# Kernel optimization log

Hardware: AMD Instinct MI355X
Metric: run time of the kernel (lower is better)

The kernel has to match this reference:

```python
import jax, jax.numpy as jnp
import numpy as np

NOT_EPSILON = 1.0
B, S, D = 1, 512, 256


def swishmax(x, axis):
    xexp = x * jnp.exp(x - jnp.max(x, axis=axis, keepdims=True))
    return xexp / (jnp.sum(jnp.abs(xexp), axis=axis, keepdims=True) + NOT_EPSILON)


def setup_inputs() -> dict:
    key = jax.random.key(0)
    ks = jax.random.split(key, 13)
    scale = 1.0 / np.sqrt(D)
    mk = lambda k: jax.random.uniform(k, (D, D), jnp.float32, -scale, scale)
    mb = lambda k: jax.random.uniform(k, (D,), jnp.float32, -scale, scale)
    return {
        "query_tokens": jax.random.normal(ks[0], (B, S, D), jnp.float32),
        "key_tokens": jax.random.normal(ks[1], (B, S, D), jnp.float32),
        "value_tokens": jax.random.normal(ks[2], (B, S, D), jnp.float32),
        "Wk": mk(ks[3]), "bk": mb(ks[4]),
        "Wq": mk(ks[5]), "bq": mb(ks[6]),
        "Wva": mk(ks[7]), "bva": mb(ks[8]),
        "Wl": mk(ks[9]), "bl": mb(ks[10]),
        "Wvo": mk(ks[11]), "bvo": mb(ks[12]),
    }


def reference(query_tokens, key_tokens, value_tokens,
              Wk, bk, Wq, bq, Wva, bva, Wl, bl, Wvo, bvo):
    # residual linear transforms of tokens
    k = key_tokens + key_tokens @ Wk + bk        # [B,S,D]
    q = query_tokens + query_tokens @ Wq + bq    # [B,S,D]
    # batchify: key -> [B,Sk,1,D], query -> [B,1,Sq,D]; outer-product scores
    attention_raw = k[:, :, None, :] * q[:, None, :, :]          # [B,Sk,Sq,D]
    attention_logits = attention_raw + attention_raw @ Wl + bl   # DxD linear on raw scores
    attention_scale = swishmax(attention_logits, axis=-2)        # normalize over query axis (dim -shape_dims)
    v = value_tokens + value_tokens @ Wva + bva  # [B,S,D]
    values_scaled = v[:, :, None, :] * attention_scale           # [B,Sk,Sq,D]
    value_sum = values_scaled.sum(axis=-3)                       # reduce key axis -> [B,Sq,D]
    value_out = value_sum + value_sum @ Wvo + bvo
    return value_out
```

## Files before the change

### kernel.cpp

```cpp
#include <hip/hip_runtime.h>
#include <math.h>

#define S_LEN 512
#define D_DIM 256
#define SLICE (S_LEN * D_DIM)

#define LOG2E  1.44269504088896f
#define LN2    0.69314718055995f
#define C2     (8.0f * LOG2E)

#define EXP2F(x) __builtin_amdgcn_exp2f(x)

typedef _Float16 half8  __attribute__((ext_vector_type(8)));
typedef _Float16 half4v __attribute__((ext_vector_type(4)));
typedef float   floatx4 __attribute__((ext_vector_type(4)));

__global__ __launch_bounds__(256) void prep_wl(const float* __restrict__ Wl,
                                               _Float16* __restrict__ WlhT)
{
    const int d = blockIdx.x, e = threadIdx.x;
    float v = (Wl[e * D_DIM + d] + (e == d ? 1.0f : 0.0f)) * LOG2E;
    WlhT[d * D_DIM + e] = (_Float16)v;
}

__global__ __launch_bounds__(256) void linres3(
    const float* __restrict__ xk, const float* __restrict__ Wk,
    const float* __restrict__ bk, _Float16* __restrict__ yk16,
    const float* __restrict__ xq, const float* __restrict__ Wq,
    const float* __restrict__ bq, _Float16* __restrict__ yq16,
    const float* __restrict__ xv, const float* __restrict__ Wv,
    const float* __restrict__ bv, float* __restrict__ yv)
{
    __shared__ float xs[4][D_DIM];
    const int r0 = blockIdx.x * 4;
    const int sel = blockIdx.y;
    const float* x = sel == 0 ? xk : (sel == 1 ? xq : xv);
    const float* W = sel == 0 ? Wk : (sel == 1 ? Wq : Wv);
    const float* b = sel == 0 ? bk : (sel == 1 ? bq : bv);

    const int tid = threadIdx.x;
    #pragma unroll
    for (int t = 0; t < 4; ++t) xs[t][tid] = x[(r0 + t) * D_DIM + tid];
    __syncthreads();
    const float bv_ = b[tid];
    float acc[4];
    #pragma unroll
    for (int i = 0; i < 4; ++i) acc[i] = xs[i][tid] + bv_;
    #pragma unroll 4
    for (int e = 0; e < D_DIM; ++e) {
        const float w = W[e * D_DIM + tid];
        #pragma unroll
        for (int i = 0; i < 4; ++i) acc[i] += xs[i][e] * w;
    }
    if (sel == 2) {
        #pragma unroll
        for (int i = 0; i < 4; ++i) yv[(r0 + i) * D_DIM + tid] = acc[i];
    } else {
        _Float16* y16 = sel == 0 ? yk16 : yq16;
        #pragma unroll
        for (int i = 0; i < 4; ++i) y16[(r0 + i) * D_DIM + tid] = (_Float16)acc[i];
    }
}

__global__ __launch_bounds__(256) void linres_sum(
    const float* __restrict__ po, const float* __restrict__ W,
    const float* __restrict__ b, float* __restrict__ y)
{
    __shared__ float xs[4][D_DIM];
    const int tid = threadIdx.x;
    const int r0  = blockIdx.x * 4;
    #pragma unroll
    for (int t = 0; t < 4; ++t) {
        float s = 0.f;
        #pragma unroll
        for (int c = 0; c < 16; ++c)
            s += po[(size_t)c * SLICE + (r0 + t) * D_DIM + tid];
        xs[t][tid] = s;
    }
    __syncthreads();
    const float bv_ = b[tid];
    float acc[4];
    #pragma unroll
    for (int i = 0; i < 4; ++i) acc[i] = xs[i][tid] + bv_;
    #pragma unroll 4
    for (int e = 0; e < D_DIM; ++e) {
        const float w = W[e * D_DIM + tid];
        #pragma unroll
        for (int i = 0; i < 4; ++i) acc[i] += xs[i][e] * w;
    }
    #pragma unroll
    for (int i = 0; i < 4; ++i) y[(r0 + i) * D_DIM + tid] = acc[i];
}

__device__ __forceinline__ void stage_q(const _Float16* __restrict__ qh,
                                        _Float16* __restrict__ Afrag,
                                        int sq0, int tid)
{
    const int i   = tid & 63;
    const int qtr = tid >> 6;
    const int mt = i >> 4, l16 = i & 15;
    const half8* src = (const half8*)(qh + (size_t)(sq0 + i) * D_DIM + qtr * 64);
    #pragma unroll
    for (int u = 0; u < 8; ++u) {
        const int eb   = qtr * 8 + u;
        const int kk   = eb >> 2, quad = eb & 3;
        const int addr16 = (mt * 8 + kk) * 64 + quad * 16 + l16;
        *(half8*)(Afrag + addr16 * 8) = src[u];
    }
}

__device__ __forceinline__ void stage_q32(const _Float16* __restrict__ qh,
                                          _Float16* __restrict__ Afrag,
                                          int sq0, int tid)
{
    const int i   = tid & 31;
    const int oct = tid >> 5;
    const int mt = i >> 4, l16 = i & 15;
    const half8* src = (const half8*)(qh + (size_t)(sq0 + i) * D_DIM);
    #pragma unroll
    for (int u = 0; u < 4; ++u) {
        const int eb   = oct * 4 + u;
        const int kk   = eb >> 2, quad = eb & 3;
        const int addr16 = (mt * 8 + kk) * 64 + quad * 16 + l16;
        *(half8*)(Afrag + addr16 * 8) = src[eb];
    }
}

__global__ __launch_bounds__(256, 2) void stats_mfma(
    const _Float16* __restrict__ qh, const _Float16* __restrict__ kh,
    const _Float16* __restrict__ WlhT, const float* __restrict__ bl,
    float* __restrict__ pm, float* __restrict__ ps)
{
    __shared__ _Float16 Afrag[32 * 64 * 8];

    const int tid  = threadIdx.x;
    const int lane = tid & 63, wave = tid >> 6;
    const int quad = lane >> 4, l16 = lane & 15;
    const int sqt  = blockIdx.x, sq0 = sqt * 64;
    const int dw   = blockIdx.y * 128 + wave * 32;
    const int sk0  = blockIdx.z * 16;

    stage_q(qh, Afrag, sq0, tid);

    half8 wl[2][8];
    #pragma unroll
    for (int nt = 0; nt < 2; ++nt) {
        const int d = dw + nt * 16 + l16;
        #pragma unroll
        for (int kk = 0; kk < 8; ++kk)
            wl[nt][kk] = *(const half8*)(WlhT + (size_t)d * D_DIM + kk * 32 + quad * 8);
    }
    float bl_r[2];
    #pragma unroll
    for (int nt = 0; nt < 2; ++nt)
        bl_r[nt] = bl[dw + nt * 16 + l16] * LOG2E;

    __syncthreads();

    #pragma unroll 1
    for (int s = 0; s < 16; ++s) {
        const int sk = sk0 + s;
        floatx4 acc[4][2];
        #pragma unroll
        for (int mt = 0; mt < 4; ++mt)
            #pragma unroll
            for (int nt = 0; nt < 2; ++nt)
                acc[mt][nt] = (floatx4){0.f, 0.f, 0.f, 0.f};

        #pragma unroll
        for (int kk = 0; kk < 8; ++kk) {
            const half8 k8 = *(const half8*)(kh + (size_t)sk * D_DIM + kk * 32 + quad * 8);
            half8 af[4], bf[2];
            #pragma unroll
            for (int mt = 0; mt < 4; ++mt)
                af[mt] = *(const half8*)(Afrag + ((mt * 8 + kk) * 64 + lane) * 8);
            #pragma unroll
            for (int nt = 0; nt < 2; ++nt)
                bf[nt] = wl[nt][kk] * k8;
            #pragma unroll
            for (int mt = 0; mt < 4; ++mt)
                #pragma unroll
                for (int nt = 0; nt < 2; ++nt)
                    acc[mt][nt] = __builtin_amdgcn_mfma_f32_16x16x32_f16(
                        af[mt], bf[nt], acc[mt][nt], 0, 0, 0);
        }

        #pragma unroll
        for (int nt = 0; nt < 2; ++nt) {
            float mmx[4], tss[4];
            #pragma unroll
            for (int mt = 0; mt < 4; ++mt) {
                float L0 = acc[mt][nt][0] + bl_r[nt];
                float L1 = acc[mt][nt][1] + bl_r[nt];
                float L2 = acc[mt][nt][2] + bl_r[nt];
                float L3 = acc[mt][nt][3] + bl_r[nt];
                float t0 = fabsf(L0) * EXP2F(L0 - C2);
                float t1 = fabsf(L1) * EXP2F(L1 - C2);
                float t2 = fabsf(L2) * EXP2F(L2 - C2);
                float t3 = fabsf(L3) * EXP2F(L3 - C2);
                mmx[mt] = fmaxf(fmaxf(L0, L1), fmaxf(L2, L3));
                tss[mt] = (t0 + t1) + (t2 + t3);
            }
            float m  = fmaxf(fmaxf(mmx[0], mmx[1]), fmaxf(mmx[2], mmx[3]));
            float ss = (tss[0] + tss[1]) + (tss[2] + tss[3]);

            #pragma unroll
            for (int mask = 16; mask <= 32; mask <<= 1) {
                m  = fmaxf(m, __shfl_xor(m, mask, 64));
                ss += __shfl_xor(ss, mask, 64);
            }
            if (quad == 0) {
                const int d = dw + nt * 16 + l16;
                pm[((size_t)sqt * S_LEN + sk) * D_DIM + d] = m;
                ps[((size_t)sqt * S_LEN + sk) * D_DIM + d] = ss;
            }
        }
    }
}

__global__ __launch_bounds__(256) void reduce_ms(
    const float* __restrict__ pm, const float* __restrict__ ps,
    const float* __restrict__ vbuf, float* __restrict__ wbuf)
{
    const int idx = blockIdx.x * 256 + threadIdx.x;
    float mv[8], sv[8];
    #pragma unroll
    for (int t = 0; t < 8; ++t) {
        mv[t] = pm[(size_t)t * SLICE + idx];
        sv[t] = ps[(size_t)t * SLICE + idx];
    }
    float M = fmaxf(fmaxf(fmaxf(mv[0], mv[1]), fmaxf(mv[2], mv[3])),
                    fmaxf(fmaxf(mv[4], mv[5]), fmaxf(mv[6], mv[7])));
    float S = ((sv[0] + sv[1]) + (sv[2] + sv[3]))
            + ((sv[4] + sv[5]) + (sv[6] + sv[7]));
    const float denom = S * LN2 + EXP2F(M - C2);
    wbuf[idx] = vbuf[idx] * (LN2 / denom);
}

__global__ __launch_bounds__(256, 2) void accum_mfma(
    const _Float16* __restrict__ qh, const _Float16* __restrict__ kh,
    const _Float16* __restrict__ WlhT, const float* __restrict__ bl,
    const float* __restrict__ wbuf, float* __restrict__ po)
{
    __shared__ _Float16 Afrag[16 * 64 * 8];

    const int tid  = threadIdx.x;
    const int lane = tid & 63, wave = tid >> 6;
    const int quad = lane >> 4, l16 = lane & 15;
    const int sq0  = blockIdx.x * 32;
    const int dw   = blockIdx.y * 128 + wave * 32;
    const int chunk = blockIdx.z;
    const int sk0  = chunk * 32;

    stage_q32(qh, Afrag, sq0, tid);

    half8 wl[2][8];
    #pragma unroll
    for (int nt = 0; nt < 2; ++nt) {
        const int d = dw + nt * 16 + l16;
        #pragma unroll
        for (int kk = 0; kk < 8; ++kk)
            wl[nt][kk] = *(const half8*)(WlhT + (size_t)d * D_DIM + kk * 32 + quad * 8);
    }
    float bl_r[2];
    #pragma unroll
    for (int nt = 0; nt < 2; ++nt)
        bl_r[nt] = bl[dw + nt * 16 + l16] * LOG2E;

    __syncthreads();

    half8 afr[2][8];
    #pragma unroll
    for (int mt = 0; mt < 2; ++mt)
        #pragma unroll
        for (int kk = 0; kk < 8; ++kk)
            afr[mt][kk] = *(const half8*)(Afrag + ((mt * 8 + kk) * 64 + lane) * 8);

    floatx4 o[2][2];
    #pragma unroll
    for (int mt = 0; mt < 2; ++mt)
        #pragma unroll
        for (int nt = 0; nt < 2; ++nt)
            o[mt][nt] = (floatx4){0.f, 0.f, 0.f, 0.f};

    #pragma unroll 1
    for (int s = 0; s < 32; ++s) {
        const int sk = sk0 + s;

        float w_r2[2];
        #pragma unroll
        for (int nt = 0; nt < 2; ++nt)
            w_r2[nt] = wbuf[(size_t)sk * D_DIM + dw + nt * 16 + l16];

        floatx4 acc[2][2];
        #pragma unroll
        for (int mt = 0; mt < 2; ++mt)
            #pragma unroll
            for (int nt = 0; nt < 2; ++nt)
                acc[mt][nt] = (floatx4){0.f, 0.f, 0.f, 0.f};

        #pragma unroll
        for (int kk = 0; kk < 8; ++kk) {
            const half8 k8 = *(const half8*)(kh + (size_t)sk * D_DIM + kk * 32 + quad * 8);
            half8 bf[2];
            #pragma unroll
            for (int nt = 0; nt < 2; ++nt)
                bf[nt] = wl[nt][kk] * k8;
            #pragma unroll
            for (int mt = 0; mt < 2; ++mt)
                #pragma unroll
                for (int nt = 0; nt < 2; ++nt)
                    acc[mt][nt] = __builtin_amdgcn_mfma_f32_16x16x32_f16(
                        afr[mt][kk], bf[nt], acc[mt][nt], 0, 0, 0);
        }

        #pragma unroll
        for (int nt = 0; nt < 2; ++nt) {
            const float w_r = w_r2[nt];
            #pragma unroll
            for (int mt = 0; mt < 2; ++mt)
                #pragma unroll
                for (int r = 0; r < 4; ++r) {
                    const float L2 = acc[mt][nt][r] + bl_r[nt];
                    o[mt][nt][r] += w_r * (L2 * EXP2F(L2 - C2));
                }
        }
    }

    float* dst = po + (size_t)chunk * SLICE;
    #pragma unroll
    for (int mt = 0; mt < 2; ++mt)
        #pragma unroll
        for (int nt = 0; nt < 2; ++nt)
            #pragma unroll
            for (int r = 0; r < 4; ++r) {
                const int row = sq0 + mt * 16 + quad * 4 + r;
                const int col = dw + nt * 16 + l16;
                dst[(size_t)row * D_DIM + col] = o[mt][nt][r];
            }
}

extern "C" void kernel_launch(void* const* d_in, const int* in_sizes, int n_in,
                              void* d_out, int out_size, void* d_ws, size_t ws_size,
                              hipStream_t stream)
{
    const float* query = (const float*)d_in[0];
    const float* key   = (const float*)d_in[1];
    const float* value = (const float*)d_in[2];
    const float* Wk  = (const float*)d_in[3];
    const float* bk  = (const float*)d_in[4];
    const float* Wq  = (const float*)d_in[5];
    const float* bq  = (const float*)d_in[6];
    const float* Wva = (const float*)d_in[7];
    const float* bva = (const float*)d_in[8];
    const float* Wl  = (const float*)d_in[9];
    const float* bl  = (const float*)d_in[10];
    const float* Wvo = (const float*)d_in[11];
    const float* bvo = (const float*)d_in[12];

    const int MAT = SLICE;
    float* ws   = (float*)d_ws;
    float* vbuf = ws + 2 * MAT;
    float* wbuf = ws + 3 * MAT;
    _Float16* WlhT = (_Float16*)(ws + 6 * MAT);
    _Float16* kh   = (_Float16*)(ws + 6 * MAT + 32768);
    _Float16* qh   = kh + MAT;
    float* pm  = ws + 6 * MAT + 32768 + 2 * 65536;
    float* ps  = pm + 8 * MAT;
    float* po  = pm;
    float* out = (float*)d_out;

    prep_wl<<<256, 256, 0, stream>>>(Wl, WlhT);
    linres3<<<dim3(128, 3), 256, 0, stream>>>(key, Wk, bk, kh,
                                              query, Wq, bq, qh,
                                              value, Wva, bva, vbuf);

    stats_mfma<<<dim3(8, 2, 32), 256, 0, stream>>>(qh, kh, WlhT, bl, pm, ps);
    reduce_ms<<<512, 256, 0, stream>>>(pm, ps, vbuf, wbuf);
    accum_mfma<<<dim3(16, 2, 16), 256, 0, stream>>>(qh, kh, WlhT, bl,
                                                    wbuf, po);

    linres_sum<<<128, 256, 0, stream>>>(po, Wvo, bvo, out);
}
```

Baseline: 216.5 us.

## Fuse Wl prep into linres3, double key rows in stats, prefetch keys in accum

Merges the separate Wl transpose/convert kernel into the linres3 launch as an extra blockIdx.y slice, removing one launch. The stats kernel now processes two key rows per iteration so each LDS query fragment is reused across twice as many MFMAs. The accum kernel software-prefetches the next key row and weight values into registers while the current row's MFMAs and exp work run. It also changes the occupancy attributes, the unroll factors, and the linres_sum tiling (2 rows per block, 256 blocks). The trade-off is higher register pressure in the MFMA kernels.

```diff
diff --git a/kernel.cpp b/kernel.cpp
--- a/kernel.cpp
+++ b/kernel.cpp
@@ -14,14 +14,6 @@
 typedef _Float16 half8  __attribute__((ext_vector_type(8)));
 typedef _Float16 half4v __attribute__((ext_vector_type(4)));
 typedef float   floatx4 __attribute__((ext_vector_type(4)));
-
-__global__ __launch_bounds__(256) void prep_wl(const float* __restrict__ Wl,
-                                               _Float16* __restrict__ WlhT)
-{
-    const int d = blockIdx.x, e = threadIdx.x;
-    float v = (Wl[e * D_DIM + d] + (e == d ? 1.0f : 0.0f)) * LOG2E;
-    WlhT[d * D_DIM + e] = (_Float16)v;
-}
 
 __global__ __launch_bounds__(256) void linres3(
     const float* __restrict__ xk, const float* __restrict__ Wk,
@@ -29,16 +21,28 @@
     const float* __restrict__ xq, const float* __restrict__ Wq,
     const float* __restrict__ bq, _Float16* __restrict__ yq16,
     const float* __restrict__ xv, const float* __restrict__ Wv,
-    const float* __restrict__ bv, float* __restrict__ yv)
-{
+    const float* __restrict__ bv, float* __restrict__ yv,
+    const float* __restrict__ Wl, _Float16* __restrict__ WlhT)
+{
+    const int tid = threadIdx.x;
+    const int sel = blockIdx.y;
+
+    if (sel == 3) {
+        #pragma unroll
+        for (int t = 0; t < 2; ++t) {
+            const int d = blockIdx.x * 2 + t;
+            float v = (Wl[tid * D_DIM + d] + (tid == d ? 1.0f : 0.0f)) * LOG2E;
+            WlhT[d * D_DIM + tid] = (_Float16)v;
+        }
+        return;
+    }
+
     __shared__ float xs[4][D_DIM];
     const int r0 = blockIdx.x * 4;
-    const int sel = blockIdx.y;
     const float* x = sel == 0 ? xk : (sel == 1 ? xq : xv);
     const float* W = sel == 0 ? Wk : (sel == 1 ? Wq : Wv);
     const float* b = sel == 0 ? bk : (sel == 1 ? bq : bv);
 
-    const int tid = threadIdx.x;
     #pragma unroll
     for (int t = 0; t < 4; ++t) xs[t][tid] = x[(r0 + t) * D_DIM + tid];
     __syncthreads();
@@ -46,7 +50,7 @@
     float acc[4];
     #pragma unroll
     for (int i = 0; i < 4; ++i) acc[i] = xs[i][tid] + bv_;
-    #pragma unroll 4
+    #pragma unroll 8
     for (int e = 0; e < D_DIM; ++e) {
         const float w = W[e * D_DIM + tid];
         #pragma unroll
@@ -66,11 +70,11 @@
     const float* __restrict__ po, const float* __restrict__ W,
     const float* __restrict__ b, float* __restrict__ y)
 {
-    __shared__ float xs[4][D_DIM];
+    __shared__ float xs[2][D_DIM];
     const int tid = threadIdx.x;
-    const int r0  = blockIdx.x * 4;
-    #pragma unroll
-    for (int t = 0; t < 4; ++t) {
+    const int r0  = blockIdx.x * 2;
+    #pragma unroll
+    for (int t = 0; t < 2; ++t) {
         float s = 0.f;
         #pragma unroll
         for (int c = 0; c < 16; ++c)
@@ -79,17 +83,17 @@
     }
     __syncthreads();
     const float bv_ = b[tid];
-    float acc[4];
-    #pragma unroll
-    for (int i = 0; i < 4; ++i) acc[i] = xs[i][tid] + bv_;
-    #pragma unroll 4
+    float acc[2];
+    #pragma unroll
+    for (int i = 0; i < 2; ++i) acc[i] = xs[i][tid] + bv_;
+    #pragma unroll 8
     for (int e = 0; e < D_DIM; ++e) {
         const float w = W[e * D_DIM + tid];
         #pragma unroll
-        for (int i = 0; i < 4; ++i) acc[i] += xs[i][e] * w;
-    }
-    #pragma unroll
-    for (int i = 0; i < 4; ++i) y[(r0 + i) * D_DIM + tid] = acc[i];
+        for (int i = 0; i < 2; ++i) acc[i] += xs[i][e] * w;
+    }
+    #pragma unroll
+    for (int i = 0; i < 2; ++i) y[(r0 + i) * D_DIM + tid] = acc[i];
 }
 
 __device__ __forceinline__ void stage_q(const _Float16* __restrict__ qh,
@@ -126,7 +130,9 @@
     }
 }
 
-__global__ __launch_bounds__(256, 2) void stats_mfma(
+__global__ __launch_bounds__(256)
+__attribute__((amdgpu_waves_per_eu(2, 2)))
+void stats_mfma(
     const _Float16* __restrict__ qh, const _Float16* __restrict__ kh,
     const _Float16* __restrict__ WlhT, const float* __restrict__ bl,
     float* __restrict__ pm, float* __restrict__ ps)
@@ -158,63 +164,71 @@
     __syncthreads();
 
     #pragma unroll 1
-    for (int s = 0; s < 16; ++s) {
-        const int sk = sk0 + s;
-        floatx4 acc[4][2];
-        #pragma unroll
-        for (int mt = 0; mt < 4; ++mt)
-            #pragma unroll
-            for (int nt = 0; nt < 2; ++nt)
-                acc[mt][nt] = (floatx4){0.f, 0.f, 0.f, 0.f};
-
-        #pragma unroll
-        for (int kk = 0; kk < 8; ++kk) {
-            const half8 k8 = *(const half8*)(kh + (size_t)sk * D_DIM + kk * 32 + quad * 8);
-            half8 af[4], bf[2];
-            #pragma unroll
-            for (int mt = 0; mt < 4; ++mt)
-                af[mt] = *(const half8*)(Afrag + ((mt * 8 + kk) * 64 + lane) * 8);
-            #pragma unroll
-            for (int nt = 0; nt < 2; ++nt)
-                bf[nt] = wl[nt][kk] * k8;
+    for (int s2 = 0; s2 < 8; ++s2) {
+        const int sk = sk0 + s2 * 2;
+
+        floatx4 acc[2][4][2];
+        #pragma unroll
+        for (int c = 0; c < 2; ++c)
             #pragma unroll
             for (int mt = 0; mt < 4; ++mt)
                 #pragma unroll
                 for (int nt = 0; nt < 2; ++nt)
-                    acc[mt][nt] = __builtin_amdgcn_mfma_f32_16x16x32_f16(
-                        af[mt], bf[nt], acc[mt][nt], 0, 0, 0);
-        }
-
-        #pragma unroll
-        for (int nt = 0; nt < 2; ++nt) {
-            float mmx[4], tss[4];
+                    acc[c][mt][nt] = (floatx4){0.f, 0.f, 0.f, 0.f};
+
+        #pragma unroll
+        for (int kk = 0; kk < 8; ++kk) {
+            const half8 k8a = *(const half8*)(kh + (size_t)sk * D_DIM + kk * 32 + quad * 8);
+            const half8 k8b = *(const half8*)(kh + (size_t)(sk + 1) * D_DIM + kk * 32 + quad * 8);
+            half8 af[4];
+            #pragma unroll
+            for (int mt = 0; mt < 4; ++mt)
+                af[mt] = *(const half8*)(Afrag + ((mt * 8 + kk) * 64 + lane) * 8);
+            const half8 bfa0 = wl[0][kk] * k8a;
+            const half8 bfa1 = wl[1][kk] * k8a;
+            const half8 bfb0 = wl[0][kk] * k8b;
+            const half8 bfb1 = wl[1][kk] * k8b;
             #pragma unroll
             for (int mt = 0; mt < 4; ++mt) {
-                float L0 = acc[mt][nt][0] + bl_r[nt];
-                float L1 = acc[mt][nt][1] + bl_r[nt];
-                float L2 = acc[mt][nt][2] + bl_r[nt];
-                float L3 = acc[mt][nt][3] + bl_r[nt];
-                float t0 = fabsf(L0) * EXP2F(L0 - C2);
-                float t1 = fabsf(L1) * EXP2F(L1 - C2);
-                float t2 = fabsf(L2) * EXP2F(L2 - C2);
-                float t3 = fabsf(L3) * EXP2F(L3 - C2);
-                mmx[mt] = fmaxf(fmaxf(L0, L1), fmaxf(L2, L3));
-                tss[mt] = (t0 + t1) + (t2 + t3);
-            }
-            float m  = fmaxf(fmaxf(mmx[0], mmx[1]), fmaxf(mmx[2], mmx[3]));
-            float ss = (tss[0] + tss[1]) + (tss[2] + tss[3]);
-
-            #pragma unroll
-            for (int mask = 16; mask <= 32; mask <<= 1) {
-                m  = fmaxf(m, __shfl_xor(m, mask, 64));
-                ss += __shfl_xor(ss, mask, 64);
-            }
-            if (quad == 0) {
-                const int d = dw + nt * 16 + l16;
-                pm[((size_t)sqt * S_LEN + sk) * D_DIM + d] = m;
-                ps[((size_t)sqt * S_LEN + sk) * D_DIM + d] = ss;
+                acc[0][mt][0] = __builtin_amdgcn_mfma_f32_16x16x32_f16(af[mt], bfa0, acc[0][mt][0], 0, 0, 0);
+                acc[0][mt][1] = __builtin_amdgcn_mfma_f32_16x16x32_f16(af[mt], bfa1, acc[0][mt][1], 0, 0, 0);
+                acc[1][mt][0] = __builtin_amdgcn_mfma_f32_16x16x32_f16(af[mt], bfb0, acc[1][mt][0], 0, 0, 0);
+                acc[1][mt][1] = __builtin_amdgcn_mfma_f32_16x16x32_f16(af[mt], bfb1, acc[1][mt][1], 0, 0, 0);
             }
         }
+
+        #pragma unroll
+        for (int c = 0; c < 2; ++c)
+            #pragma unroll
+            for (int nt = 0; nt < 2; ++nt) {
+                float mmx[4], tss[4];
+                #pragma unroll
+                for (int mt = 0; mt < 4; ++mt) {
+                    float L0 = acc[c][mt][nt][0] + bl_r[nt];
+                    float L1 = acc[c][mt][nt][1] + bl_r[nt];
+                    float L2 = acc[c][mt][nt][2] + bl_r[nt];
+                    float L3 = acc[c][mt][nt][3] + bl_r[nt];
+                    float t0 = fabsf(L0) * EXP2F(L0 - C2);
+                    float t1 = fabsf(L1) * EXP2F(L1 - C2);
+                    float t2 = fabsf(L2) * EXP2F(L2 - C2);
+                    float t3 = fabsf(L3) * EXP2F(L3 - C2);
+                    mmx[mt] = fmaxf(fmaxf(L0, L1), fmaxf(L2, L3));
+                    tss[mt] = (t0 + t1) + (t2 + t3);
+                }
+                float m  = fmaxf(fmaxf(mmx[0], mmx[1]), fmaxf(mmx[2], mmx[3]));
+                float ss = (tss[0] + tss[1]) + (tss[2] + tss[3]);
+
+                #pragma unroll
+                for (int mask = 16; mask <= 32; mask <<= 1) {
+                    m  = fmaxf(m, __shfl_xor(m, mask, 64));
+                    ss += __shfl_xor(ss, mask, 64);
+                }
+                if (quad == 0) {
+                    const int d = dw + nt * 16 + l16;
+                    pm[((size_t)sqt * S_LEN + sk + c) * D_DIM + d] = m;
+                    ps[((size_t)sqt * S_LEN + sk + c) * D_DIM + d] = ss;
+                }
+            }
     }
 }
 
@@ -237,7 +251,9 @@
     wbuf[idx] = vbuf[idx] * (LN2 / denom);
 }
 
-__global__ __launch_bounds__(256, 2) void accum_mfma(
+__global__ __launch_bounds__(256)
+__attribute__((amdgpu_waves_per_eu(2, 2)))
+void accum_mfma(
     const _Float16* __restrict__ qh, const _Float16* __restrict__ kh,
     const _Float16* __restrict__ WlhT, const float* __restrict__ bl,
     const float* __restrict__ wbuf, float* __restrict__ po)
@@ -283,15 +299,17 @@
         for (int nt = 0; nt < 2; ++nt)
             o[mt][nt] = (floatx4){0.f, 0.f, 0.f, 0.f};
 
+    half8 k8c[8];
+    #pragma unroll
+    for (int kk = 0; kk < 8; ++kk)
+        k8c[kk] = *(const half8*)(kh + (size_t)sk0 * D_DIM + kk * 32 + quad * 8);
+    float w_c0 = wbuf[(size_t)sk0 * D_DIM + dw + l16];
+    float w_c1 = wbuf[(size_t)sk0 * D_DIM + dw + 16 + l16];
+
     #pragma unroll 1
     for (int s = 0; s < 32; ++s) {
         const int sk = sk0 + s;
 
-        float w_r2[2];
-        #pragma unroll
-        for (int nt = 0; nt < 2; ++nt)
-            w_r2[nt] = wbuf[(size_t)sk * D_DIM + dw + nt * 16 + l16];
-
         floatx4 acc[2][2];
         #pragma unroll
         for (int mt = 0; mt < 2; ++mt)
@@ -301,30 +319,32 @@
 
         #pragma unroll
         for (int kk = 0; kk < 8; ++kk) {
-            const half8 k8 = *(const half8*)(kh + (size_t)sk * D_DIM + kk * 32 + quad * 8);
-            half8 bf[2];
-            #pragma unroll
-            for (int nt = 0; nt < 2; ++nt)
-                bf[nt] = wl[nt][kk] * k8;
-            #pragma unroll
-            for (int mt = 0; mt < 2; ++mt)
-                #pragma unroll
-                for (int nt = 0; nt < 2; ++nt)
-                    acc[mt][nt] = __builtin_amdgcn_mfma_f32_16x16x32_f16(
-                        afr[mt][kk], bf[nt], acc[mt][nt], 0, 0, 0);
+            const half8 bf0 = wl[0][kk] * k8c[kk];
+            const half8 bf1 = wl[1][kk] * k8c[kk];
+            acc[0][0] = __builtin_amdgcn_mfma_f32_16x16x32_f16(afr[0][kk], bf0, acc[0][0], 0, 0, 0);
+            acc[0][1] = __builtin_amdgcn_mfma_f32_16x16x32_f16(afr[0][kk], bf1, acc[0][1], 0, 0, 0);
+            acc[1][0] = __builtin_amdgcn_mfma_f32_16x16x32_f16(afr[1][kk], bf0, acc[1][0], 0, 0, 0);
+            acc[1][1] = __builtin_amdgcn_mfma_f32_16x16x32_f16(afr[1][kk], bf1, acc[1][1], 0, 0, 0);
         }
 
-        #pragma unroll
-        for (int nt = 0; nt < 2; ++nt) {
-            const float w_r = w_r2[nt];
-            #pragma unroll
-            for (int mt = 0; mt < 2; ++mt)
-                #pragma unroll
-                for (int r = 0; r < 4; ++r) {
-                    const float L2 = acc[mt][nt][r] + bl_r[nt];
-                    o[mt][nt][r] += w_r * (L2 * EXP2F(L2 - C2));
-                }
+        const float w_use0 = w_c0, w_use1 = w_c1;
+        if (s < 31) {
+            #pragma unroll
+            for (int kk = 0; kk < 8; ++kk)
+                k8c[kk] = *(const half8*)(kh + (size_t)(sk + 1) * D_DIM + kk * 32 + quad * 8);
+            w_c0 = wbuf[(size_t)(sk + 1) * D_DIM + dw + l16];
+            w_c1 = wbuf[(size_t)(sk + 1) * D_DIM + dw + 16 + l16];
         }
+
+        #pragma unroll
+        for (int mt = 0; mt < 2; ++mt)
+            #pragma unroll
+            for (int r = 0; r < 4; ++r) {
+                const float La = acc[mt][0][r] + bl_r[0];
+                const float Lb = acc[mt][1][r] + bl_r[1];
+                o[mt][0][r] += w_use0 * (La * EXP2F(La - C2));
+                o[mt][1][r] += w_use1 * (Lb * EXP2F(Lb - C2));
+            }
     }
 
     float* dst = po + (size_t)chunk * SLICE;
@@ -370,15 +390,15 @@
     float* po  = pm;
     float* out = (float*)d_out;
 
-    prep_wl<<<256, 256, 0, stream>>>(Wl, WlhT);
-    linres3<<<dim3(128, 3), 256, 0, stream>>>(key, Wk, bk, kh,
+    linres3<<<dim3(128, 4), 256, 0, stream>>>(key, Wk, bk, kh,
                                               query, Wq, bq, qh,
-                                              value, Wva, bva, vbuf);
+                                              value, Wva, bva, vbuf,
+                                              Wl, WlhT);
 
     stats_mfma<<<dim3(8, 2, 32), 256, 0, stream>>>(qh, kh, WlhT, bl, pm, ps);
     reduce_ms<<<512, 256, 0, stream>>>(pm, ps, vbuf, wbuf);
     accum_mfma<<<dim3(16, 2, 16), 256, 0, stream>>>(qh, kh, WlhT, bl,
                                                     wbuf, po);
 
-    linres_sum<<<128, 256, 0, stream>>>(po, Wvo, bvo, out);
-}
+    linres_sum<<<256, 256, 0, stream>>>(po, Wvo, bvo, out);
+}
```

Result: faster. 210.0 us (-3.0%).
